# Performance work log

Measured on AMD Instinct MI355X. Metric: run time of the kernel, lower is better.

The kernel has to match this reference:

```python
import jax, jax.numpy as jnp
import numpy as np

D_MODEL = 1024
NHEAD = 16
DIM_HEAD = 64
SCALE = DIM_HEAD ** (-0.5)


def setup_inputs() -> dict:
    key = jax.random.key(0)
    ks = jax.random.split(key, 8)
    B, N = 2, 2048
    inner = NHEAD * DIM_HEAD
    s = 0.02
    return {
        "query": jax.random.normal(ks[0], (B, N, D_MODEL), jnp.float32),
        "key": jax.random.normal(ks[1], (B, N, D_MODEL), jnp.float32),
        "value": jax.random.normal(ks[2], (B, N, D_MODEL), jnp.float32),
        "Wq": jax.random.normal(ks[3], (D_MODEL, inner), jnp.float32) * s,
        "Wk": jax.random.normal(ks[4], (D_MODEL, inner), jnp.float32) * s,
        "Wv": jax.random.normal(ks[5], (D_MODEL, inner), jnp.float32) * s,
        "Wo": jax.random.normal(ks[6], (inner, D_MODEL), jnp.float32) * s,
        "bo": jnp.zeros((D_MODEL,), jnp.float32),
    }


def reference(query, key, value, Wq, Wk, Wv, Wo, bo):
    B, Nq, _ = query.shape
    Nk = key.shape[1]
    # projections (no bias), split heads: [B, N, h, d]
    q = (query @ Wq).reshape(B, Nq, NHEAD, DIM_HEAD)
    k = (key @ Wk).reshape(B, Nk, NHEAD, DIM_HEAD)
    v = (value @ Wv).reshape(B, Nk, NHEAD, DIM_HEAD)
    # scores [B, h, Nq, Nk]
    sim = jnp.einsum('bihd,bjhd->bhij', q, k) * SCALE
    attn = jax.nn.softmax(sim, axis=-1)  # dropout p=0.0 -> identity
    out = jnp.einsum('bhij,bjhd->bihd', attn, v).reshape(B, Nq, NHEAD * DIM_HEAD)
    return out @ Wo + bo
```

## Files before the change

kernel.cpp:

```cpp
#include <hip/hip_runtime.h>
#include <stdint.h>

typedef __attribute__((ext_vector_type(8))) short short8;
typedef __attribute__((ext_vector_type(8))) unsigned short ushort8;
typedef __attribute__((ext_vector_type(4))) unsigned short ushort4v;
typedef __attribute__((ext_vector_type(4))) float float4v;
typedef _Float16 half4v __attribute__((ext_vector_type(4)));

#define D_MODEL 1024
#define NHEAD 16
#define DIM_HEAD 64
#define BATCH 2
#define SEQ 2048
#define BH (BATCH*NHEAD)
#define MROWS (BATCH*SEQ)
#define MK ((size_t)MROWS * D_MODEL)

__device__ __forceinline__ unsigned short f2bf(float f) {
  union { float f; unsigned u; } v; v.f = f;
  unsigned r = v.u + 0x7fffu + ((v.u >> 16) & 1u);
  return (unsigned short)(r >> 16);
}
__device__ __forceinline__ unsigned short f2bf_fast(float f) {
  union { float f; unsigned u; } v; v.f = f;
  return (unsigned short)((v.u + 0x8000u) >> 16);
}
__device__ __forceinline__ unsigned pk2bf(float a, float b) {
  union { float f; unsigned u; } x, y; x.f = a; y.f = b;
  return __builtin_amdgcn_perm(y.u + 0x8000u, x.u + 0x8000u, 0x07060302u);
}

__device__ __forceinline__ void gld16(const unsigned short* g, unsigned short* l) {
  __builtin_amdgcn_global_load_lds(
      (const __attribute__((address_space(1))) unsigned int*)g,
      (__attribute__((address_space(3))) unsigned int*)l, 16, 0, 0);
}

__global__ __launch_bounds__(256) void wtrans_kernel(const float* __restrict__ Wq,
    const float* __restrict__ Wk, const float* __restrict__ Wv,
    const float* __restrict__ Wo, unsigned short* __restrict__ WT0) {
  __shared__ float tile[32][33];
  const int z = blockIdx.z;
  const float* W = (z == 0) ? Wq : (z == 1) ? Wk : (z == 2) ? Wv : Wo;
  const float scale = (z == 0) ? 0.125f : 1.0f;
  unsigned short* WT = WT0 + ((size_t)z << 20);
  int bn = blockIdx.x * 32;
  int bk = blockIdx.y * 32;
  int tx = threadIdx.x & 31, ty = threadIdx.x >> 5;
#pragma unroll
  for (int i = 0; i < 4; i++)
    tile[ty + i*8][tx] = W[(size_t)(bk + ty + i*8) * D_MODEL + bn + tx];
  __syncthreads();
#pragma unroll
  for (int i = 0; i < 4; i++)
    WT[(size_t)(bn + ty + i*8) * D_MODEL + bk + tx] = f2bf(tile[tx][ty + i*8] * scale);
}

__global__ __launch_bounds__(256) void cast_kernel(const float* __restrict__ q,
    const float* __restrict__ k, const float* __restrict__ v,
    unsigned short* __restrict__ out) {
  const float* src = (blockIdx.y == 0) ? q : (blockIdx.y == 1) ? k : v;
  unsigned short* dst = out + (size_t)blockIdx.y * MK;
  size_t idx = ((size_t)blockIdx.x * 256 + threadIdx.x) * 8;
  float4v a = *(const float4v*)(src + idx);
  float4v b = *(const float4v*)(src + idx + 4);
  ushort8 o;
  o[0] = f2bf(a[0]); o[1] = f2bf(a[1]); o[2] = f2bf(a[2]); o[3] = f2bf(a[3]);
  o[4] = f2bf(b[0]); o[5] = f2bf(b[1]); o[6] = f2bf(b[2]); o[7] = f2bf(b[3]);
  *(ushort8*)(dst + idx) = o;
}

__global__ __launch_bounds__(256) void vtrans_kernel(const unsigned short* __restrict__ Vb,
                                                     unsigned short* __restrict__ VT) {
  __shared__ unsigned short tile[64][72];
  const int bh = blockIdx.x;
  const int b = bh >> 4, h = bh & 15;
  const int n0 = blockIdx.y * 64;
  const int t = threadIdx.x;
#pragma unroll
  for (int p = 0; p < 2; p++) {
    int g = p*256 + t; int row = g >> 3, c = g & 7;
    *(ushort8*)&tile[row][c*8] =
      *(const ushort8*)(Vb + ((size_t)((b*SEQ + n0 + row)*NHEAD + h))*DIM_HEAD + c*8);
  }
  __syncthreads();
  int d = t >> 2, kc = (t & 3) * 16;
  ushort8 o0, o1;
#pragma unroll
  for (int j = 0; j < 8; j++) { o0[j] = tile[kc + j][d]; o1[j] = tile[kc + 8 + j][d]; }
  unsigned short* dst = VT + ((size_t)(bh*DIM_HEAD + d))*SEQ + n0 + kc;
  *(ushort8*)dst = o0;
  *(ushort8*)(dst + 8) = o1;
}

__global__ __launch_bounds__(256, 3) void proj_kernel(const unsigned short* __restrict__ Xbf,
    const unsigned short* __restrict__ WT0, unsigned short* __restrict__ Y0) {
  __shared__ unsigned short Al[128*64];
  __shared__ unsigned short Bl[128*64];
  const int z = blockIdx.z;
  const unsigned short* A  = Xbf + (size_t)z * MK;
  const unsigned short* BT = WT0 + ((size_t)z << 20);
  unsigned short* Y = Y0 + (size_t)z * MK;
  const int m0 = blockIdx.x * 128, n0 = blockIdx.y * 128;
  const int t = threadIdx.x;
  const int lane = t & 63, w = t >> 6, quad = lane >> 4, lid = lane & 15;
  const int wm = w & 1, wn = w >> 1;
  const int r8 = lane >> 3, c8 = (lane & 7) * 8;

  float4v acc[4][4];
#pragma unroll
  for (int i = 0; i < 4; i++)
#pragma unroll
    for (int j = 0; j < 4; j++) acc[i][j] = (float4v)0.0f;

  for (int k0 = 0; k0 < D_MODEL; k0 += 64) {
#pragma unroll
    for (int p = 0; p < 4; p++) {
      int seg = w*4 + p;
      gld16(A  + (size_t)(m0 + seg*8 + r8) * D_MODEL + k0 + c8, &Al[seg*8*64]);
      gld16(BT + (size_t)(n0 + seg*8 + r8) * D_MODEL + k0 + c8, &Bl[seg*8*64]);
    }
    __syncthreads();
#pragma unroll
    for (int kst = 0; kst < 2; kst++) {
      short8 af[4], bfr[4];
#pragma unroll
      for (int i = 0; i < 4; i++)
        af[i] = *(const short8*)&Al[(wm*64 + i*16 + lid)*64 + kst*32 + quad*8];
#pragma unroll
      for (int j = 0; j < 4; j++)
        bfr[j] = *(const short8*)&Bl[(wn*64 + j*16 + lid)*64 + kst*32 + quad*8];
#pragma unroll
      for (int i = 0; i < 4; i++)
#pragma unroll
        for (int j = 0; j < 4; j++)
          acc[i][j] = __builtin_amdgcn_mfma_f32_16x16x32_bf16(af[i], bfr[j], acc[i][j], 0, 0, 0);
    }
    __syncthreads();
  }
#pragma unroll
  for (int i = 0; i < 4; i++)
#pragma unroll
    for (int j = 0; j < 4; j++)
#pragma unroll
      for (int r = 0; r < 4; r++) {
        int row = m0 + wm*64 + i*16 + quad*4 + r;
        int col = n0 + wn*64 + j*16 + lid;
        Y[(size_t)row * D_MODEL + col] = f2bf_fast(acc[i][j][r]);
      }
}

__global__ __launch_bounds__(256, 3) void outproj_kernel(const unsigned short* __restrict__ A,
    const unsigned short* __restrict__ WT, const float* __restrict__ bias,
    float* __restrict__ out) {
  __shared__ unsigned short Al[64*64];
  __shared__ unsigned short Bl[128*64];
  const int m0 = blockIdx.x * 64, n0 = blockIdx.y * 128;
  const int t = threadIdx.x;
  const int lane = t & 63, w = t >> 6, quad = lane >> 4, lid = lane & 15;
  const int wm = w & 1, wn = w >> 1;
  const int r8 = lane >> 3, c8 = (lane & 7) * 8;

  float4v acc[2][4];
#pragma unroll
  for (int i = 0; i < 2; i++)
#pragma unroll
    for (int j = 0; j < 4; j++) acc[i][j] = (float4v)0.0f;

  for (int k0 = 0; k0 < D_MODEL; k0 += 64) {
#pragma unroll
    for (int p = 0; p < 2; p++) {
      int seg = w*2 + p;
      gld16(A + (size_t)(m0 + seg*8 + r8) * D_MODEL + k0 + c8, &Al[seg*8*64]);
    }
#pragma unroll
    for (int p = 0; p < 4; p++) {
      int seg = w*4 + p;
      gld16(WT + (size_t)(n0 + seg*8 + r8) * D_MODEL + k0 + c8, &Bl[seg*8*64]);
    }
    __syncthreads();
#pragma unroll
    for (int kst = 0; kst < 2; kst++) {
      short8 af[2], bfr[4];
#pragma unroll
      for (int i = 0; i < 2; i++)
        af[i] = *(const short8*)&Al[(wm*32 + i*16 + lid)*64 + kst*32 + quad*8];
#pragma unroll
      for (int j = 0; j < 4; j++)
        bfr[j] = *(const short8*)&Bl[(wn*64 + j*16 + lid)*64 + kst*32 + quad*8];
#pragma unroll
      for (int i = 0; i < 2; i++)
#pragma unroll
        for (int j = 0; j < 4; j++)
          acc[i][j] = __builtin_amdgcn_mfma_f32_16x16x32_bf16(af[i], bfr[j], acc[i][j], 0, 0, 0);
    }
    __syncthreads();
  }
#pragma unroll
  for (int i = 0; i < 2; i++)
#pragma unroll
    for (int j = 0; j < 4; j++)
#pragma unroll
      for (int r = 0; r < 4; r++) {
        int row = m0 + wm*32 + i*16 + quad*4 + r;
        int col = n0 + wn*64 + j*16 + lid;
        out[(size_t)row * D_MODEL + col] = acc[i][j][r] + bias[col];
      }
}

#define QB 128
#define KB 64
#define FSTR 72
#define PSTR 68

__global__ __launch_bounds__(256, 4) void flash_kernel(const unsigned short* __restrict__ Q,
    const unsigned short* __restrict__ K, const unsigned short* __restrict__ VT,
    _Float16* __restrict__ Op0, _Float16* __restrict__ Op1,
    float* __restrict__ lpart) {
  __shared__ unsigned short Ql[QB][FSTR];
  __shared__ unsigned short Kl[KB][FSTR];
  __shared__ unsigned short Vt[DIM_HEAD][FSTR];

  const int bh = blockIdx.x;
  const int b = bh >> 4, h = bh & 15;
  const int q0 = blockIdx.y * QB;
  const int z = blockIdx.z;
  const int kbeg = z * (SEQ/2);
  const int t = threadIdx.x;
  const int lane = t & 63, w = t >> 6, quad = lane >> 4, lid = lane & 15;
  _Float16* Op = z ? Op1 : Op0;
  float* lp = lpart + (size_t)z * BH * SEQ;
  unsigned short* Ptw = &Ql[0][0] + w * 16 * PSTR;

  {
#pragma unroll
    for (int p = 0; p < 4; p++) {
      int g = p*256 + t; int row = g >> 3, c = g & 7;
      *(ushort8*)&Ql[row][c*8] =
        *(const ushort8*)(Q + ((size_t)((b*SEQ + q0 + row)*NHEAD + h))*DIM_HEAD + c*8);
    }
  }
  __syncthreads();
  short8 qf[2][2];
#pragma unroll
  for (int st = 0; st < 2; st++)
#pragma unroll
    for (int kst = 0; kst < 2; kst++)
      qf[st][kst] = *(const short8*)&Ql[w*32 + st*16 + lid][kst*32 + quad*8];

  float4v o[2][4];
#pragma unroll
  for (int st = 0; st < 2; st++)
#pragma unroll
    for (int i = 0; i < 4; i++) o[st][i] = (float4v)0.0f;
  float ps[2] = {0.0f, 0.0f};

  for (int kb = kbeg; kb < kbeg + SEQ/2; kb += KB) {
    {
#pragma unroll
      for (int p = 0; p < 2; p++) {
        int g = p*256 + t; int row = g >> 3, c = g & 7;
        *(ushort8*)&Kl[row][c*8] =
          *(const ushort8*)(K + ((size_t)((b*SEQ + kb + row)*NHEAD + h))*DIM_HEAD + c*8);
        *(ushort8*)&Vt[row][c*8] =
          *(const ushort8*)(VT + ((size_t)(bh*DIM_HEAD + row))*SEQ + kb + c*8);
      }
    }
    __syncthreads();

    float4v s[2][4];
#pragma unroll
    for (int st = 0; st < 2; st++)
#pragma unroll
      for (int mb = 0; mb < 4; mb++) s[st][mb] = (float4v)0.0f;
#pragma unroll
    for (int kst = 0; kst < 2; kst++)
#pragma unroll
      for (int mb = 0; mb < 4; mb++) {
        short8 kf = *(const short8*)&Kl[mb*16 + lid][kst*32 + quad*8];
        s[0][mb] = __builtin_amdgcn_mfma_f32_16x16x32_bf16(kf, qf[0][kst], s[0][mb], 0, 0, 0);
        s[1][mb] = __builtin_amdgcn_mfma_f32_16x16x32_bf16(kf, qf[1][kst], s[1][mb], 0, 0, 0);
      }

    short8 pf[2][2];
#pragma unroll
    for (int st = 0; st < 2; st++) {
#pragma unroll
      for (int mb = 0; mb < 4; mb++) {
        float e0 = __expf(s[st][mb][0]);
        float e1 = __expf(s[st][mb][1]);
        float e2 = __expf(s[st][mb][2]);
        float e3 = __expf(s[st][mb][3]);
        ps[st] += (e0 + e1) + (e2 + e3);
        uint2 pk; pk.x = pk2bf(e0, e1); pk.y = pk2bf(e2, e3);
        *(uint2*)&Ptw[lid*PSTR + mb*16 + quad*4] = pk;
      }
      pf[st][0] = *(const short8*)&Ptw[lid*PSTR + quad*8];
      pf[st][1] = *(const short8*)&Ptw[lid*PSTR + 32 + quad*8];
    }

#pragma unroll
    for (int kst = 0; kst < 2; kst++)
#pragma unroll
      for (int i = 0; i < 4; i++) {
        short8 vf = *(const short8*)&Vt[i*16 + lid][kst*32 + quad*8];
        o[0][i] = __builtin_amdgcn_mfma_f32_16x16x32_bf16(vf, pf[0][kst], o[0][i], 0, 0, 0);
        o[1][i] = __builtin_amdgcn_mfma_f32_16x16x32_bf16(vf, pf[1][kst], o[1][i], 0, 0, 0);
      }
    __syncthreads();
  }

#pragma unroll
  for (int st = 0; st < 2; st++) {
    float v = ps[st];
    v += __shfl_xor(v, 16); v += __shfl_xor(v, 32);
    int q = q0 + w*32 + st*16 + lid;
    if (quad == 0) lp[(size_t)bh*SEQ + q] = v;
#pragma unroll
    for (int i = 0; i < 4; i++) {
      half4v hv;
#pragma unroll
      for (int r = 0; r < 4; r++) hv[r] = (_Float16)o[st][i][r];
      *(half4v*)(Op + ((size_t)bh*SEQ + q)*64 + i*16 + quad*4) = hv;
    }
  }
}

__global__ __launch_bounds__(256) void norm_kernel(const _Float16* __restrict__ Op0,
    const _Float16* __restrict__ Op1, const float* __restrict__ lpart,
    unsigned short* __restrict__ Ob) {
  int g = blockIdx.x * 256 + threadIdx.x;
  int d4 = g & 15, h = (g >> 4) & 15, q = (g >> 8) & (SEQ - 1), b = g >> 19;
  int bh = b * NHEAD + h;
  size_t obase = ((size_t)bh * SEQ + q) * 64 + d4 * 4;
  half4v a = *(const half4v*)(Op0 + obase);
  half4v c = *(const half4v*)(Op1 + obase);
  float l = lpart[(size_t)bh*SEQ + q] + lpart[(size_t)BH*SEQ + (size_t)bh*SEQ + q];
  float inv = 1.0f / l;
  float f0 = ((float)a[0] + (float)c[0]) * inv;
  float f1 = ((float)a[1] + (float)c[1]) * inv;
  float f2 = ((float)a[2] + (float)c[2]) * inv;
  float f3 = ((float)a[3] + (float)c[3]) * inv;
  uint2 pk; pk.x = pk2bf(f0, f1); pk.y = pk2bf(f2, f3);
  *(uint2*)&Ob[(((size_t)(b*SEQ + q))*NHEAD + h)*64 + d4*4] = pk;
}

extern "C" void kernel_launch(void* const* d_in, const int* in_sizes, int n_in,
                              void* d_out, int out_size, void* d_ws, size_t ws_size,
                              hipStream_t stream) {
  const float* query = (const float*)d_in[0];
  const float* key_  = (const float*)d_in[1];
  const float* value = (const float*)d_in[2];
  const float* Wq = (const float*)d_in[3];
  const float* Wk = (const float*)d_in[4];
  const float* Wv = (const float*)d_in[5];
  const float* Wo = (const float*)d_in[6];
  const float* bo = (const float*)d_in[7];
  float* out = (float*)d_out;

  char* ws = (char*)d_ws;
  unsigned short* WT0 = (unsigned short*)(ws);
  unsigned short* Xbf = (unsigned short*)(ws + (8ll  << 20));
  unsigned short* VT  = (unsigned short*)(ws + (8ll  << 20));
  unsigned short* Ob  = (unsigned short*)(ws + (16ll << 20));
  _Float16*       Op0 = (_Float16*)     (ws + (24ll << 20));
  unsigned short* Qb  = (unsigned short*)(ws + (32ll << 20));
  unsigned short* Kb  = (unsigned short*)(ws + (40ll << 20));
  unsigned short* Vb  = (unsigned short*)(ws + (48ll << 20));
  _Float16*       Op1 = (_Float16*)     (ws + (56ll << 20));
  float*          lp  = (float*)        (ws + (64ll << 20));

  dim3 tb(256);
  dim3 tg(32, 32, 4);
  hipLaunchKernelGGL(wtrans_kernel, tg, tb, 0, stream, Wq, Wk, Wv, Wo, WT0);

  dim3 cg(MK / (256*8), 3);
  hipLaunchKernelGGL(cast_kernel, cg, tb, 0, stream, query, key_, value, Xbf);

  dim3 pg(MROWS/128, D_MODEL/128, 3);
  hipLaunchKernelGGL(proj_kernel, pg, tb, 0, stream, Xbf, WT0, Qb);

  dim3 vg(BH, SEQ/64);
  hipLaunchKernelGGL(vtrans_kernel, vg, tb, 0, stream, Vb, VT);

  dim3 fg(BH, SEQ/QB, 2);
  hipLaunchKernelGGL(flash_kernel, fg, tb, 0, stream, Qb, Kb, VT, Op0, Op1, lp);

  dim3 ng((MROWS * NHEAD * DIM_HEAD / 4) / 256);
  hipLaunchKernelGGL(norm_kernel, ng, tb, 0, stream, Op0, Op1, lp, Ob);

  dim3 og(MROWS/64, D_MODEL/128);
  hipLaunchKernelGGL(outproj_kernel, og, tb, 0, stream, Ob, WT0 + (3ll << 20), bo, out);
}
```

Measured before the change: 245.3 us.

## Load K/V fragments directly from global in flash kernel, drop LDS staging and barriers

The flash attention kernel no longer stages Q, K and V^T tiles in shared memory with block-wide barriers. Each wave now loads its MFMA fragments straight from global memory and handles 64 query rows (four 16-row subtiles), with only a small per-wave LDS buffer for the P transpose. The grid is flattened to 512 blocks with a head-interleaved index mapping, and launch bounds drop to 2 blocks per CU to leave room for the larger register footprint. This removes __syncthreads and LDS traffic, but each wave repeats the K/V global loads (relying on L2/L1 reuse) and occupancy falls.

```diff
diff --git a/kernel.cpp b/kernel.cpp
--- a/kernel.cpp
+++ b/kernel.cpp
@@ -208,113 +208,93 @@
       }
 }
 
-#define QB 128
-#define KB 64
-#define FSTR 72
 #define PSTR 68
 
-__global__ __launch_bounds__(256, 4) void flash_kernel(const unsigned short* __restrict__ Q,
+__global__ __launch_bounds__(256, 2) void flash_kernel(const unsigned short* __restrict__ Q,
     const unsigned short* __restrict__ K, const unsigned short* __restrict__ VT,
     _Float16* __restrict__ Op0, _Float16* __restrict__ Op1,
     float* __restrict__ lpart) {
-  __shared__ unsigned short Ql[QB][FSTR];
-  __shared__ unsigned short Kl[KB][FSTR];
-  __shared__ unsigned short Vt[DIM_HEAD][FSTR];
-
-  const int bh = blockIdx.x;
+  __shared__ unsigned short Pl[4][4][16*PSTR];
+
+  const int flat = blockIdx.x;
+  const int bh  = (flat & 7) * 4 + ((flat >> 3) & 3);
+  const int qz  = flat >> 5;
+  const int qb  = qz & 7, z = qz >> 3;
   const int b = bh >> 4, h = bh & 15;
-  const int q0 = blockIdx.y * QB;
-  const int z = blockIdx.z;
-  const int kbeg = z * (SEQ/2);
   const int t = threadIdx.x;
   const int lane = t & 63, w = t >> 6, quad = lane >> 4, lid = lane & 15;
+  const int q0 = qb * 256 + w * 64;
+  const int kbeg = z * (SEQ/2);
   _Float16* Op = z ? Op1 : Op0;
   float* lp = lpart + (size_t)z * BH * SEQ;
-  unsigned short* Ptw = &Ql[0][0] + w * 16 * PSTR;
-
-  {
-#pragma unroll
-    for (int p = 0; p < 4; p++) {
-      int g = p*256 + t; int row = g >> 3, c = g & 7;
-      *(ushort8*)&Ql[row][c*8] =
-        *(const ushort8*)(Q + ((size_t)((b*SEQ + q0 + row)*NHEAD + h))*DIM_HEAD + c*8);
-    }
-  }
-  __syncthreads();
-  short8 qf[2][2];
-#pragma unroll
-  for (int st = 0; st < 2; st++)
+
+  short8 qf[4][2];
+#pragma unroll
+  for (int st = 0; st < 4; st++)
 #pragma unroll
     for (int kst = 0; kst < 2; kst++)
-      qf[st][kst] = *(const short8*)&Ql[w*32 + st*16 + lid][kst*32 + quad*8];
-
-  float4v o[2][4];
-#pragma unroll
-  for (int st = 0; st < 2; st++)
+      qf[st][kst] = *(const short8*)(Q +
+        ((size_t)((b*SEQ + q0 + st*16 + lid)*NHEAD + h))*DIM_HEAD + kst*32 + quad*8);
+
+  float4v o[4][4];
+#pragma unroll
+  for (int st = 0; st < 4; st++)
 #pragma unroll
     for (int i = 0; i < 4; i++) o[st][i] = (float4v)0.0f;
-  float ps[2] = {0.0f, 0.0f};
-
-  for (int kb = kbeg; kb < kbeg + SEQ/2; kb += KB) {
-    {
-#pragma unroll
-      for (int p = 0; p < 2; p++) {
-        int g = p*256 + t; int row = g >> 3, c = g & 7;
-        *(ushort8*)&Kl[row][c*8] =
-          *(const ushort8*)(K + ((size_t)((b*SEQ + kb + row)*NHEAD + h))*DIM_HEAD + c*8);
-        *(ushort8*)&Vt[row][c*8] =
-          *(const ushort8*)(VT + ((size_t)(bh*DIM_HEAD + row))*SEQ + kb + c*8);
-      }
-    }
-    __syncthreads();
-
-    float4v s[2][4];
-#pragma unroll
-    for (int st = 0; st < 2; st++)
-#pragma unroll
-      for (int mb = 0; mb < 4; mb++) s[st][mb] = (float4v)0.0f;
+  float ps[4] = {0.0f, 0.0f, 0.0f, 0.0f};
+
+  for (int kb = kbeg; kb < kbeg + SEQ/2; kb += 64) {
+    short8 kf[2][4], vf[2][4];
 #pragma unroll
     for (int kst = 0; kst < 2; kst++)
 #pragma unroll
+      for (int mb = 0; mb < 4; mb++)
+        kf[kst][mb] = *(const short8*)(K +
+          ((size_t)((b*SEQ + kb + mb*16 + lid)*NHEAD + h))*DIM_HEAD + kst*32 + quad*8);
+#pragma unroll
+    for (int kst = 0; kst < 2; kst++)
+#pragma unroll
+      for (int i = 0; i < 4; i++)
+        vf[kst][i] = *(const short8*)(VT +
+          ((size_t)(bh*DIM_HEAD + i*16 + lid))*SEQ + kb + kst*32 + quad*8);
+
+#pragma unroll
+    for (int st = 0; st < 4; st++) {
+      float4v s[4];
+#pragma unroll
+      for (int mb = 0; mb < 4; mb++) s[mb] = (float4v)0.0f;
+#pragma unroll
+      for (int kst = 0; kst < 2; kst++)
+#pragma unroll
+        for (int mb = 0; mb < 4; mb++)
+          s[mb] = __builtin_amdgcn_mfma_f32_16x16x32_bf16(kf[kst][mb], qf[st][kst], s[mb], 0, 0, 0);
+
+      unsigned short* Ptw = &Pl[w][st][0];
+#pragma unroll
       for (int mb = 0; mb < 4; mb++) {
-        short8 kf = *(const short8*)&Kl[mb*16 + lid][kst*32 + quad*8];
-        s[0][mb] = __builtin_amdgcn_mfma_f32_16x16x32_bf16(kf, qf[0][kst], s[0][mb], 0, 0, 0);
-        s[1][mb] = __builtin_amdgcn_mfma_f32_16x16x32_bf16(kf, qf[1][kst], s[1][mb], 0, 0, 0);
-      }
-
-    short8 pf[2][2];
-#pragma unroll
-    for (int st = 0; st < 2; st++) {
-#pragma unroll
-      for (int mb = 0; mb < 4; mb++) {
-        float e0 = __expf(s[st][mb][0]);
-        float e1 = __expf(s[st][mb][1]);
-        float e2 = __expf(s[st][mb][2]);
-        float e3 = __expf(s[st][mb][3]);
+        float e0 = __expf(s[mb][0]);
+        float e1 = __expf(s[mb][1]);
+        float e2 = __expf(s[mb][2]);
+        float e3 = __expf(s[mb][3]);
         ps[st] += (e0 + e1) + (e2 + e3);
         uint2 pk; pk.x = pk2bf(e0, e1); pk.y = pk2bf(e2, e3);
         *(uint2*)&Ptw[lid*PSTR + mb*16 + quad*4] = pk;
       }
-      pf[st][0] = *(const short8*)&Ptw[lid*PSTR + quad*8];
-      pf[st][1] = *(const short8*)&Ptw[lid*PSTR + 32 + quad*8];
-    }
-
-#pragma unroll
-    for (int kst = 0; kst < 2; kst++)
+      short8 pf0 = *(const short8*)&Ptw[lid*PSTR + quad*8];
+      short8 pf1 = *(const short8*)&Ptw[lid*PSTR + 32 + quad*8];
 #pragma unroll
       for (int i = 0; i < 4; i++) {
-        short8 vf = *(const short8*)&Vt[i*16 + lid][kst*32 + quad*8];
-        o[0][i] = __builtin_amdgcn_mfma_f32_16x16x32_bf16(vf, pf[0][kst], o[0][i], 0, 0, 0);
-        o[1][i] = __builtin_amdgcn_mfma_f32_16x16x32_bf16(vf, pf[1][kst], o[1][i], 0, 0, 0);
+        o[st][i] = __builtin_amdgcn_mfma_f32_16x16x32_bf16(vf[0][i], pf0, o[st][i], 0, 0, 0);
+        o[st][i] = __builtin_amdgcn_mfma_f32_16x16x32_bf16(vf[1][i], pf1, o[st][i], 0, 0, 0);
       }
-    __syncthreads();
-  }
-
-#pragma unroll
-  for (int st = 0; st < 2; st++) {
+    }
+  }
+
+#pragma unroll
+  for (int st = 0; st < 4; st++) {
     float v = ps[st];
     v += __shfl_xor(v, 16); v += __shfl_xor(v, 32);
-    int q = q0 + w*32 + st*16 + lid;
+    int q = q0 + st*16 + lid;
     if (quad == 0) lp[(size_t)bh*SEQ + q] = v;
 #pragma unroll
     for (int i = 0; i < 4; i++) {
@@ -383,7 +363,7 @@
   dim3 vg(BH, SEQ/64);
   hipLaunchKernelGGL(vtrans_kernel, vg, tb, 0, stream, Vb, VT);
 
-  dim3 fg(BH, SEQ/QB, 2);
+  dim3 fg(512);
   hipLaunchKernelGGL(flash_kernel, fg, tb, 0, stream, Qb, Kb, VT, Op0, Op1, lp);
 
   dim3 ng((MROWS * NHEAD * DIM_HEAD / 4) / 256);
```

Result: no change. 245.7 us (+0.2%).
